# Kernel optimization log

Measured on AMD Instinct MI355X. Metric: run time of the kernel, lower is better.

The kernel has to match this reference:

```python
import jax, jax.numpy as jnp
import numpy as np

NUM_LAYERS = 4

def setup_inputs() -> dict:
    key = jax.random.key(0)
    x = jax.random.normal(key, (4000000, 9), dtype=jnp.float32)
    return {"x": x}

def reference(x) -> jnp.ndarray:
    # reshape to batched 3x3 matrices
    xm = x.reshape(-1, 3, 3)
    # Frobenius norm per matrix, keepdims for broadcast
    norm = jnp.sqrt(jnp.sum(xm * xm, axis=(1, 2), keepdims=True))
    Q = xm / norm
    for _ in range(NUM_LAYERS):
        # N = Q^T Q  (b33)
        N = jnp.einsum('bji,bjk->bik', Q, Q)
        P = 0.5 * jnp.einsum('bij,bjk->bik', Q, N)
        Q = 2.0 * Q + jnp.einsum('bij,bjk->bik', P, N) - 3.0 * P
    return Q.reshape(x.shape)
```

## Files before the change

kernel.cpp:

```cpp
#include <hip/hip_runtime.h>


#define NLAYERS 4

typedef float v4f __attribute__((ext_vector_type(4)));

__global__ __launch_bounds__(256) void
proj_kernel(const float* __restrict__ x, float* __restrict__ out) {
    __shared__ float lin[256 * 9];
    __shared__ float lout[256 * 9];
    const int tid = threadIdx.x;
    const long long mbase = (long long)blockIdx.x * 256;

    const v4f* __restrict__ gin = (const v4f*)(x + mbase * 9);
    v4f* lin4 = (v4f*)lin;
    lin4[tid]       = gin[tid];
    lin4[tid + 256] = gin[tid + 256];
    if (tid < 64) lin4[tid + 512] = gin[tid + 512];
    __syncthreads();

    float q[9];
#pragma unroll
    for (int k = 0; k < 9; ++k) q[k] = lin[tid * 9 + k];

    float s = 0.f;
#pragma unroll
    for (int k = 0; k < 9; ++k) s = __builtin_fmaf(q[k], q[k], s);
    const float inv = rsqrtf(s);
#pragma unroll
    for (int k = 0; k < 9; ++k) q[k] *= inv;

#pragma unroll
    for (int layer = 0; layer < NLAYERS; ++layer) {
        const float n00 = q[0]*q[0] + q[3]*q[3] + q[6]*q[6];
        const float n01 = q[0]*q[1] + q[3]*q[4] + q[6]*q[7];
        const float n02 = q[0]*q[2] + q[3]*q[5] + q[6]*q[8];
        const float n11 = q[1]*q[1] + q[4]*q[4] + q[7]*q[7];
        const float n12 = q[1]*q[2] + q[4]*q[5] + q[7]*q[8];
        const float n22 = q[2]*q[2] + q[5]*q[5] + q[8]*q[8];

        const float a00 = __builtin_fmaf(0.5f, n00, -1.5f);
        const float a11 = __builtin_fmaf(0.5f, n11, -1.5f);
        const float a22 = __builtin_fmaf(0.5f, n22, -1.5f);
        const float a01 = 0.5f * n01;
        const float a02 = 0.5f * n02;
        const float a12 = 0.5f * n12;

        const float m00 = __builtin_fmaf(a00,n00, __builtin_fmaf(a01,n01, __builtin_fmaf(a02,n02, 2.0f)));
        const float m01 = __builtin_fmaf(a00,n01, __builtin_fmaf(a01,n11, a02*n12));
        const float m02 = __builtin_fmaf(a00,n02, __builtin_fmaf(a01,n12, a02*n22));
        const float m11 = __builtin_fmaf(a01,n01, __builtin_fmaf(a11,n11, __builtin_fmaf(a12,n12, 2.0f)));
        const float m12 = __builtin_fmaf(a01,n02, __builtin_fmaf(a11,n12, a12*n22));
        const float m22 = __builtin_fmaf(a02,n02, __builtin_fmaf(a12,n12, __builtin_fmaf(a22,n22, 2.0f)));

        const float M[3][3] = {{m00, m01, m02}, {m01, m11, m12}, {m02, m12, m22}};

        float qn[9];
#pragma unroll
        for (int i = 0; i < 3; ++i)
#pragma unroll
            for (int j = 0; j < 3; ++j)
                qn[3*i+j] = __builtin_fmaf(q[3*i+0], M[0][j],
                            __builtin_fmaf(q[3*i+1], M[1][j],
                                           q[3*i+2] * M[2][j]));
#pragma unroll
        for (int k = 0; k < 9; ++k) q[k] = qn[k];
    }

#pragma unroll
    for (int k = 0; k < 9; ++k) lout[tid * 9 + k] = q[k];
    __syncthreads();

    v4f* __restrict__ gout = (v4f*)(out + mbase * 9);
    const v4f* lout4 = (const v4f*)lout;
    __builtin_nontemporal_store(lout4[tid],       gout + tid);
    __builtin_nontemporal_store(lout4[tid + 256], gout + tid + 256);
    if (tid < 64)
        __builtin_nontemporal_store(lout4[tid + 512], gout + tid + 512);
}

extern "C" void kernel_launch(void* const* d_in, const int* in_sizes, int n_in,
                              void* d_out, int out_size, void* d_ws, size_t ws_size,
                              hipStream_t stream) {
    const float* x = (const float*)d_in[0];
    float* out = (float*)d_out;
    const int nmat = in_sizes[0] / 9;
    const int blocks = nmat / 256;
    proj_kernel<<<blocks, 256, 0, stream>>>(x, out);
}
```

Measured before the change: 245.9 us.

## Process four matrices per thread and store outputs directly as 16-byte vectors

Each thread now handles four consecutive matrices (36 floats, nine float4s). Input still goes through shared memory, but outputs are written straight from registers as nine contiguous nontemporal float4 stores, so the output LDS staging buffer and the second barrier are gone. The aim is to cut the block count and the per-matrix LDS and barrier overhead. In exchange it uses four times the shared memory per block and more registers, which lowers occupancy. Per-thread 144-byte strided global stores coalesce worse, and the tail is handled only when nmat is a multiple of four.

```diff
diff --git a/kernel.cpp b/kernel.cpp
--- a/kernel.cpp
+++ b/kernel.cpp
@@ -2,81 +2,96 @@
 
 
 #define NLAYERS 4
+#define MPT 4
 
 typedef float v4f __attribute__((ext_vector_type(4)));
 
 __global__ __launch_bounds__(256) void
-proj_kernel(const float* __restrict__ x, float* __restrict__ out) {
-    __shared__ float lin[256 * 9];
-    __shared__ float lout[256 * 9];
+proj_kernel(const float* __restrict__ x, float* __restrict__ out,
+            int n_active_threads, int total_f4) {
+    __shared__ float lin[256 * 9 * MPT];
     const int tid = threadIdx.x;
-    const long long mbase = (long long)blockIdx.x * 256;
+    const long long t_global = (long long)blockIdx.x * 256 + tid;
+    const long long bb4 = (long long)blockIdx.x * (256 * 9);
 
-    const v4f* __restrict__ gin = (const v4f*)(x + mbase * 9);
+    const v4f* __restrict__ gin = (const v4f*)x;
     v4f* lin4 = (v4f*)lin;
-    lin4[tid]       = gin[tid];
-    lin4[tid + 256] = gin[tid + 256];
-    if (tid < 64) lin4[tid + 512] = gin[tid + 512];
+#pragma unroll
+    for (int j = 0; j < 9; ++j) {
+        const long long idx = bb4 + tid + 256 * j;
+        if (idx < total_f4) lin4[tid + 256 * j] = gin[idx];
+    }
     __syncthreads();
 
-    float q[9];
+    if (t_global >= n_active_threads) return;
+
+    float buf[9 * MPT];
+    {
+        v4f* b4 = (v4f*)buf;
+        const v4f* src = (const v4f*)(lin + tid * (9 * MPT));
 #pragma unroll
-    for (int k = 0; k < 9; ++k) q[k] = lin[tid * 9 + k];
-
-    float s = 0.f;
-#pragma unroll
-    for (int k = 0; k < 9; ++k) s = __builtin_fmaf(q[k], q[k], s);
-    const float inv = rsqrtf(s);
-#pragma unroll
-    for (int k = 0; k < 9; ++k) q[k] *= inv;
-
-#pragma unroll
-    for (int layer = 0; layer < NLAYERS; ++layer) {
-        const float n00 = q[0]*q[0] + q[3]*q[3] + q[6]*q[6];
-        const float n01 = q[0]*q[1] + q[3]*q[4] + q[6]*q[7];
-        const float n02 = q[0]*q[2] + q[3]*q[5] + q[6]*q[8];
-        const float n11 = q[1]*q[1] + q[4]*q[4] + q[7]*q[7];
-        const float n12 = q[1]*q[2] + q[4]*q[5] + q[7]*q[8];
-        const float n22 = q[2]*q[2] + q[5]*q[5] + q[8]*q[8];
-
-        const float a00 = __builtin_fmaf(0.5f, n00, -1.5f);
-        const float a11 = __builtin_fmaf(0.5f, n11, -1.5f);
-        const float a22 = __builtin_fmaf(0.5f, n22, -1.5f);
-        const float a01 = 0.5f * n01;
-        const float a02 = 0.5f * n02;
-        const float a12 = 0.5f * n12;
-
-        const float m00 = __builtin_fmaf(a00,n00, __builtin_fmaf(a01,n01, __builtin_fmaf(a02,n02, 2.0f)));
-        const float m01 = __builtin_fmaf(a00,n01, __builtin_fmaf(a01,n11, a02*n12));
-        const float m02 = __builtin_fmaf(a00,n02, __builtin_fmaf(a01,n12, a02*n22));
-        const float m11 = __builtin_fmaf(a01,n01, __builtin_fmaf(a11,n11, __builtin_fmaf(a12,n12, 2.0f)));
-        const float m12 = __builtin_fmaf(a01,n02, __builtin_fmaf(a11,n12, a12*n22));
-        const float m22 = __builtin_fmaf(a02,n02, __builtin_fmaf(a12,n12, __builtin_fmaf(a22,n22, 2.0f)));
-
-        const float M[3][3] = {{m00, m01, m02}, {m01, m11, m12}, {m02, m12, m22}};
-
-        float qn[9];
-#pragma unroll
-        for (int i = 0; i < 3; ++i)
-#pragma unroll
-            for (int j = 0; j < 3; ++j)
-                qn[3*i+j] = __builtin_fmaf(q[3*i+0], M[0][j],
-                            __builtin_fmaf(q[3*i+1], M[1][j],
-                                           q[3*i+2] * M[2][j]));
-#pragma unroll
-        for (int k = 0; k < 9; ++k) q[k] = qn[k];
+        for (int j = 0; j < 9; ++j) b4[j] = src[j];
     }
 
 #pragma unroll
-    for (int k = 0; k < 9; ++k) lout[tid * 9 + k] = q[k];
-    __syncthreads();
+    for (int m = 0; m < MPT; ++m) {
+        float q[9];
+#pragma unroll
+        for (int k = 0; k < 9; ++k) q[k] = buf[9 * m + k];
 
-    v4f* __restrict__ gout = (v4f*)(out + mbase * 9);
-    const v4f* lout4 = (const v4f*)lout;
-    __builtin_nontemporal_store(lout4[tid],       gout + tid);
-    __builtin_nontemporal_store(lout4[tid + 256], gout + tid + 256);
-    if (tid < 64)
-        __builtin_nontemporal_store(lout4[tid + 512], gout + tid + 512);
+        float s = 0.f;
+#pragma unroll
+        for (int k = 0; k < 9; ++k) s = __builtin_fmaf(q[k], q[k], s);
+        const float inv = rsqrtf(s);
+#pragma unroll
+        for (int k = 0; k < 9; ++k) q[k] *= inv;
+
+#pragma unroll
+        for (int layer = 0; layer < NLAYERS; ++layer) {
+            const float n00 = q[0]*q[0] + q[3]*q[3] + q[6]*q[6];
+            const float n01 = q[0]*q[1] + q[3]*q[4] + q[6]*q[7];
+            const float n02 = q[0]*q[2] + q[3]*q[5] + q[6]*q[8];
+            const float n11 = q[1]*q[1] + q[4]*q[4] + q[7]*q[7];
+            const float n12 = q[1]*q[2] + q[4]*q[5] + q[7]*q[8];
+            const float n22 = q[2]*q[2] + q[5]*q[5] + q[8]*q[8];
+
+            const float a00 = __builtin_fmaf(0.5f, n00, -1.5f);
+            const float a11 = __builtin_fmaf(0.5f, n11, -1.5f);
+            const float a22 = __builtin_fmaf(0.5f, n22, -1.5f);
+            const float a01 = 0.5f * n01;
+            const float a02 = 0.5f * n02;
+            const float a12 = 0.5f * n12;
+
+            const float m00 = __builtin_fmaf(a00,n00, __builtin_fmaf(a01,n01, __builtin_fmaf(a02,n02, 2.0f)));
+            const float m01 = __builtin_fmaf(a00,n01, __builtin_fmaf(a01,n11, a02*n12));
+            const float m02 = __builtin_fmaf(a00,n02, __builtin_fmaf(a01,n12, a02*n22));
+            const float m11 = __builtin_fmaf(a01,n01, __builtin_fmaf(a11,n11, __builtin_fmaf(a12,n12, 2.0f)));
+            const float m12 = __builtin_fmaf(a01,n02, __builtin_fmaf(a11,n12, a12*n22));
+            const float m22 = __builtin_fmaf(a02,n02, __builtin_fmaf(a12,n12, __builtin_fmaf(a22,n22, 2.0f)));
+
+            const float M[3][3] = {{m00, m01, m02}, {m01, m11, m12}, {m02, m12, m22}};
+
+            float qn[9];
+#pragma unroll
+            for (int i = 0; i < 3; ++i)
+#pragma unroll
+                for (int j = 0; j < 3; ++j)
+                    qn[3*i+j] = __builtin_fmaf(q[3*i+0], M[0][j],
+                                __builtin_fmaf(q[3*i+1], M[1][j],
+                                               q[3*i+2] * M[2][j]));
+#pragma unroll
+            for (int k = 0; k < 9; ++k) q[k] = qn[k];
+        }
+
+#pragma unroll
+        for (int k = 0; k < 9; ++k) buf[9 * m + k] = q[k];
+    }
+
+    v4f* __restrict__ dst = (v4f*)(out + t_global * (9 * MPT));
+    const v4f* b4 = (const v4f*)buf;
+#pragma unroll
+    for (int j = 0; j < 9; ++j)
+        __builtin_nontemporal_store(b4[j], dst + j);
 }
 
 extern "C" void kernel_launch(void* const* d_in, const int* in_sizes, int n_in,
@@ -85,6 +100,8 @@
     const float* x = (const float*)d_in[0];
     float* out = (float*)d_out;
     const int nmat = in_sizes[0] / 9;
-    const int blocks = nmat / 256;
-    proj_kernel<<<blocks, 256, 0, stream>>>(x, out);
+    const int n_active = nmat / MPT;
+    const int total_f4 = (nmat * 9) / 4;
+    const int blocks = (n_active + 255) / 256;
+    proj_kernel<<<blocks, 256, 0, stream>>>(x, out, n_active, total_f4);
 }
```

Result: slower. 501.6 us (+104.0%).
